# Kernel tuning notes

Measured on AMD Instinct MI355X. Metric: run time of the kernel, lower is better.

The kernel has to match this reference:

```python
import jax, jax.numpy as jnp
import numpy as np

LEAKY_SLOPE = 0.2  # PyG GATConv default negative_slope
EPS = 1e-16


def _gat_layer(h_in, src, dst, W, a_src, a_dst, b, concat):
    # h_in: [N, Fin]; src/dst: [Etot] (self-loops included); W: [Fin, H*C]
    N = h_in.shape[0]
    H, C = a_src.shape
    h = (h_in @ W).reshape(N, H, C)                       # [N,H,C]
    al_s = jnp.sum(h * a_src, axis=-1)                    # [N,H]
    al_d = jnp.sum(h * a_dst, axis=-1)                    # [N,H]
    e = jax.nn.leaky_relu(al_s[src] + al_d[dst], LEAKY_SLOPE)  # [E,H]
    emax = jax.ops.segment_max(e, dst, num_segments=N)    # segment softmax over dst
    p = jnp.exp(e - emax[dst])
    denom = jax.ops.segment_sum(p, dst, num_segments=N)
    alpha = p / (denom[dst] + EPS)                        # [E,H]
    out = jax.ops.segment_sum(h[src] * alpha[:, :, None], dst, num_segments=N)  # [N,H,C]
    out = out.reshape(N, H * C) if concat else out.mean(axis=1)
    return out + b


def setup_inputs() -> dict:
    key = jax.random.key(0)
    ks = jax.random.split(key, 16)
    N, E, Fin, Hd, Hh = 10000, 320000, 256, 128, 4

    def glorot(k, shape, fan_in):
        return jax.random.normal(k, shape, dtype=jnp.float32) * (1.0 / np.sqrt(fan_in))

    inp = {
        "x": jax.random.normal(ks[0], (N, Fin), dtype=jnp.float32),
        "edge_index": jax.random.randint(ks[1], (2, E), 0, N, dtype=jnp.int32),
        # conv1: Fin -> Hd x Hh heads, concat
        "W1": glorot(ks[2], (Fin, Hh * Hd), Fin),
        "a1_src": glorot(ks[3], (Hh, Hd), Hd),
        "a1_dst": glorot(ks[4], (Hh, Hd), Hd),
        "b1": jnp.zeros((Hh * Hd,), jnp.float32),
        # conv2: Hh*Hd -> Hd x Hh heads, concat
        "W2": glorot(ks[5], (Hh * Hd, Hh * Hd), Hh * Hd),
        "a2_src": glorot(ks[6], (Hh, Hd), Hd),
        "a2_dst": glorot(ks[7], (Hh, Hd), Hd),
        "b2": jnp.zeros((Hh * Hd,), jnp.float32),
        # conv3: Hh*Hd -> Hd, 1 head, concat=False (mean)
        "W3": glorot(ks[8], (Hh * Hd, Hd), Hh * Hd),
        "a3_src": glorot(ks[9], (1, Hd), Hd),
        "a3_dst": glorot(ks[10], (1, Hd), Hd),
        "b3": jnp.zeros((Hd,), jnp.float32),
        # classifier: Hd -> Hd//2 -> 2
        "Wc1": glorot(ks[11], (Hd, Hd // 2), Hd),
        "bc1": jnp.zeros((Hd // 2,), jnp.float32),
        "Wc2": glorot(ks[12], (Hd // 2, 2), Hd // 2),
        "bc2": jnp.zeros((2,), jnp.float32),
    }
    return inp


def reference(x, edge_index, W1, a1_src, a1_dst, b1, W2, a2_src, a2_dst, b2,
              W3, a3_src, a3_dst, b3, Wc1, bc1, Wc2, bc2):
    N = x.shape[0]
    loops = jnp.arange(N, dtype=edge_index.dtype)
    src = jnp.concatenate([edge_index[0], loops])  # PyG adds self-loops
    dst = jnp.concatenate([edge_index[1], loops])

    h = jax.nn.elu(_gat_layer(x, src, dst, W1, a1_src, a1_dst, b1, concat=True))
    h = jax.nn.elu(_gat_layer(h, src, dst, W2, a2_src, a2_dst, b2, concat=True))
    embeddings = _gat_layer(h, src, dst, W3, a3_src, a3_dst, b3, concat=False)  # [N, 128]
    out = jax.nn.relu(embeddings @ Wc1 + bc1) @ Wc2 + bc2  # [N, 2]
    return out, embeddings
```

## Files before the change

### kernel.cpp

```cpp
#include <hip/hip_runtime.h>
#include <cstddef>

#define LEAKY 0.2f
#define EPS_DEN 1e-16f

typedef short bf8_t __attribute__((ext_vector_type(8)));
typedef float f4_t __attribute__((ext_vector_type(4)));
typedef unsigned short us2_t __attribute__((ext_vector_type(2)));

__device__ __forceinline__ unsigned short f2bf(float f) {
    unsigned u = __float_as_uint(f);
    unsigned r = (u + 0x7fffu + ((u >> 16) & 1u)) >> 16;
    return (unsigned short)r;
}
__device__ __forceinline__ float bf2f(unsigned short h) {
    return __uint_as_float(((unsigned)h) << 16);
}

__global__ void hist_kernel(const int* __restrict__ dst, int* __restrict__ counts, int E) {
    int i = blockIdx.x * blockDim.x + threadIdx.x;
    if (i < E) atomicAdd(&counts[dst[i]], 1);
}

__global__ void scan1_kernel(int* __restrict__ cnt, int* __restrict__ bsum, int N) {
    __shared__ int s[256];
    int t = threadIdx.x;
    int i = blockIdx.x * 256 + t;
    int v = (i < N) ? cnt[i] : 0;
    s[t] = v;
    __syncthreads();
#pragma unroll
    for (int st = 1; st < 256; st <<= 1) {
        int add = (t >= st) ? s[t - st] : 0;
        __syncthreads();
        s[t] += add;
        __syncthreads();
    }
    if (i < N) cnt[i] = s[t] - v;
    if (t == 255) bsum[blockIdx.x] = s[255];
}

__global__ void scan2_kernel(int* __restrict__ bsum, int* __restrict__ offs, int NB, int N) {
    int t = threadIdx.x;
    int v = (t < NB) ? bsum[t] : 0;
    int inc = v;
#pragma unroll
    for (int off = 1; off < 64; off <<= 1) {
        int u = __shfl_up(inc, off);
        if (t >= off) inc += u;
    }
    if (t < NB) bsum[t] = inc - v;
    if (t == 63) offs[N] = inc;
}

__global__ void scan3_kernel(int* __restrict__ cnt, const int* __restrict__ bsum,
                             int* __restrict__ offs, int N) {
    int i = blockIdx.x * 256 + threadIdx.x;
    if (i < N) {
        int o = cnt[i] + bsum[blockIdx.x];
        offs[i] = o;
        cnt[i] = o;
    }
}

__global__ void scatter_kernel(const int* __restrict__ src, const int* __restrict__ dst,
                               int* __restrict__ cursor, int* __restrict__ csrc, int E) {
    int i = blockIdx.x * blockDim.x + threadIdx.x;
    if (i < E) {
        int d = dst[i];
        int pos = atomicAdd(&cursor[d], 1);
        csrc[pos] = src[i];
    }
}

__global__ void split_kernel(const float* __restrict__ in, unsigned short* __restrict__ hi,
                             unsigned short* __restrict__ lo, int len) {
    int i = blockIdx.x * blockDim.x + threadIdx.x;
    if (i >= len) return;
    float v = in[i];
    unsigned short h = f2bf(v);
    hi[i] = h;
    lo[i] = f2bf(v - bf2f(h));
}

__global__ void wsplit_kernel(const float* __restrict__ W, unsigned short* __restrict__ hi,
                              unsigned short* __restrict__ lo, int K, int N) {
    int idx = blockIdx.x * blockDim.x + threadIdx.x;
    if (idx >= K * N) return;
    int n = idx / K, k = idx % K;
    float v = W[(size_t)k * N + n];
    unsigned short h = f2bf(v);
    hi[idx] = h;
    lo[idx] = f2bf(v - bf2f(h));
}

__global__ __launch_bounds__(256) void mfma_gemm_kernel(
    const unsigned short* __restrict__ Ahi, const unsigned short* __restrict__ Alo,
    const unsigned short* __restrict__ BThi, const unsigned short* __restrict__ BTlo,
    float* __restrict__ C, int M, int N, int K) {
    constexpr int BK = 32;
    __shared__ __align__(16) unsigned short sA[128 * BK];
    __shared__ __align__(16) unsigned short sB[128 * BK];
    int t = threadIdx.x;
    int w = t >> 6, lane = t & 63;
    int quad = lane >> 4, low = lane & 15;
    int m0 = blockIdx.y * 128, n0 = blockIdx.x * 128;
    int wm = (w & 1) * 64, wn = (w >> 1) * 64;

    f4_t acc[4][4];
#pragma unroll
    for (int i = 0; i < 4; i++)
#pragma unroll
        for (int j = 0; j < 4; j++) acc[i][j] = (f4_t){0.f, 0.f, 0.f, 0.f};

    int srow = lane >> 2;
    int schunk = lane & 3;

    const unsigned short* Ap[3] = {Ahi, Ahi, Alo};
    const unsigned short* Bp[3] = {BThi, BTlo, BThi};

    for (int pass = 0; pass < 3; pass++) {
        const unsigned short* A = Ap[pass];
        const unsigned short* B = Bp[pass];
        for (int k0 = 0; k0 < K; k0 += BK) {
            __syncthreads();
#pragma unroll
            for (int inst = 0; inst < 2; inst++) {
                int r = w * 32 + inst * 16 + srow;
                int gm = m0 + r;
                if (gm >= M) gm = M - 1;
                const void* g = (const void*)(A + (size_t)gm * K + k0 + schunk * 8);
                void* l = (void*)((char*)sA + (size_t)(w * 2048 + inst * 1024));
                __builtin_amdgcn_global_load_lds((const __attribute__((address_space(1))) void*)g,
                                                 (__attribute__((address_space(3))) void*)l, 16, 0, 0);
            }
#pragma unroll
            for (int inst = 0; inst < 2; inst++) {
                int r = w * 32 + inst * 16 + srow;
                int gn = n0 + r;
                const void* g = (const void*)(B + (size_t)gn * K + k0 + schunk * 8);
                void* l = (void*)((char*)sB + (size_t)(w * 2048 + inst * 1024));
                __builtin_amdgcn_global_load_lds((const __attribute__((address_space(1))) void*)g,
                                                 (__attribute__((address_space(3))) void*)l, 16, 0, 0);
            }
            __syncthreads();

            bf8_t af[4], bf[4];
#pragma unroll
            for (int i = 0; i < 4; i++) {
                int row = wm + i * 16 + low;
                af[i] = *(const bf8_t*)&sA[row * BK + quad * 8];
            }
#pragma unroll
            for (int j = 0; j < 4; j++) {
                int row = wn + j * 16 + low;
                bf[j] = *(const bf8_t*)&sB[row * BK + quad * 8];
            }
#pragma unroll
            for (int i = 0; i < 4; i++)
#pragma unroll
                for (int j = 0; j < 4; j++)
                    acc[i][j] = __builtin_amdgcn_mfma_f32_16x16x32_bf16(af[i], bf[j], acc[i][j], 0, 0, 0);
        }
    }

#pragma unroll
    for (int i = 0; i < 4; i++) {
#pragma unroll
        for (int r = 0; r < 4; r++) {
            int gm = m0 + wm + i * 16 + quad * 4 + r;
            if (gm >= M) continue;
#pragma unroll
            for (int j = 0; j < 4; j++) {
                int gn = n0 + wn + j * 16 + low;
                C[(size_t)gm * N + gn] = acc[i][j][r];
            }
        }
    }
}

__global__ void al_h4_kernel(const float* __restrict__ h, const float* __restrict__ a_src,
                             const float* __restrict__ a_dst, float* __restrict__ als,
                             float* __restrict__ ald, int N) {
    int wave = threadIdx.x >> 6, lane = threadIdx.x & 63;
    int n = blockIdx.x * 4 + wave;
    if (n >= N) return;
    const float* row = h + (size_t)n * 512;
    float ps[4] = {0, 0, 0, 0}, pd[4] = {0, 0, 0, 0};
#pragma unroll
    for (int k = 0; k < 8; k++) {
        int f = k * 64 + lane;
        float v = row[f];
        ps[k >> 1] += v * a_src[f];
        pd[k >> 1] += v * a_dst[f];
    }
#pragma unroll
    for (int off = 32; off; off >>= 1) {
#pragma unroll
        for (int hd = 0; hd < 4; hd++) {
            ps[hd] += __shfl_down(ps[hd], off);
            pd[hd] += __shfl_down(pd[hd], off);
        }
    }
    if (lane == 0) {
#pragma unroll
        for (int hd = 0; hd < 4; hd++) {
            als[n * 4 + hd] = ps[hd];
            ald[n * 4 + hd] = pd[hd];
        }
    }
}

__global__ void al_h1_kernel(const float* __restrict__ h, const float* __restrict__ a_src,
                             const float* __restrict__ a_dst, float* __restrict__ als,
                             float* __restrict__ ald, int N) {
    int wave = threadIdx.x >> 6, lane = threadIdx.x & 63;
    int n = blockIdx.x * 4 + wave;
    if (n >= N) return;
    const float* row = h + (size_t)n * 128;
    float v0 = row[lane], v1 = row[lane + 64];
    float ps = v0 * a_src[lane] + v1 * a_src[lane + 64];
    float pd = v0 * a_dst[lane] + v1 * a_dst[lane + 64];
#pragma unroll
    for (int off = 32; off; off >>= 1) {
        ps += __shfl_down(ps, off);
        pd += __shfl_down(pd, off);
    }
    if (lane == 0) { als[n] = ps; ald[n] = pd; }
}

__global__ void stats_h4_kernel(const int* __restrict__ csrc, const int* __restrict__ offs,
                                const float* __restrict__ als, const float* __restrict__ ald,
                                float* __restrict__ pbuf, float* __restrict__ psf, int N, int E) {
    int wave = threadIdx.x >> 6, lane = threadIdx.x & 63;
    int n = blockIdx.x * 4 + wave;
    if (n >= N) return;
    int hd = lane & 3, es = lane >> 2;
    float aldn = ald[n * 4 + hd];
    float selfe = als[n * 4 + hd] + aldn;
    selfe = selfe > 0.f ? selfe : LEAKY * selfe;
    int beg = offs[n], end = offs[n + 1];
    float* pb = pbuf + (size_t)hd * E;
    float m = selfe;
    for (int base = beg; base + es < end; base += 16) {
        int idx = base + es;
        int s = csrc[idx];
        float e = als[s * 4 + hd] + aldn;
        e = e > 0.f ? e : LEAKY * e;
        pb[idx] = e;
        m = fmaxf(m, e);
    }
#pragma unroll
    for (int off = 4; off < 64; off <<= 1) m = fmaxf(m, __shfl_xor(m, off));
    float d = 0.f;
    for (int base = beg; base + es < end; base += 16) {
        int idx = base + es;
        float p = __expf(pb[idx] - m);
        pb[idx] = p;
        d += p;
    }
#pragma unroll
    for (int off = 4; off < 64; off <<= 1) d += __shfl_xor(d, off);
    float pself = __expf(selfe - m);
    float r = 1.0f / (d + pself + EPS_DEN);
    if (es == 0) psf[n * 4 + hd] = pself * r;
    for (int base = beg; base + es < end; base += 16) {
        int idx = base + es;
        pb[idx] *= r;
    }
}

__global__ void stats_h1_kernel(const int* __restrict__ csrc, const int* __restrict__ offs,
                                const float* __restrict__ als, const float* __restrict__ ald,
                                float* __restrict__ pbuf, float* __restrict__ psf, int N) {
    int wave = threadIdx.x >> 6, lane = threadIdx.x & 63;
    int n = blockIdx.x * 4 + wave;
    if (n >= N) return;
    float aldn = ald[n];
    float selfe = als[n] + aldn;
    selfe = selfe > 0.f ? selfe : LEAKY * selfe;
    int beg = offs[n], end = offs[n + 1];
    float m = selfe;
    for (int base = beg; base + lane < end; base += 64) {
        int idx = base + lane;
        int s = csrc[idx];
        float e = als[s] + aldn;
        e = e > 0.f ? e : LEAKY * e;
        pbuf[idx] = e;
        m = fmaxf(m, e);
    }
#pragma unroll
    for (int off = 1; off < 64; off <<= 1) m = fmaxf(m, __shfl_xor(m, off));
    float d = 0.f;
    for (int base = beg; base + lane < end; base += 64) {
        int idx = base + lane;
        float p = __expf(pbuf[idx] - m);
        pbuf[idx] = p;
        d += p;
    }
#pragma unroll
    for (int off = 1; off < 64; off <<= 1) d += __shfl_xor(d, off);
    float pself = __expf(selfe - m);
    float r = 1.0f / (d + pself + EPS_DEN);
    if (lane == 0) psf[n] = pself * r;
    for (int base = beg; base + lane < end; base += 64) {
        int idx = base + lane;
        pbuf[idx] *= r;
    }
}

template <bool DO_ELU>
__global__ __launch_bounds__(64) void gat_aggregate_h4_kernel(
    const float* __restrict__ h, const float* __restrict__ pbuf,
    const float* __restrict__ psf, const int* __restrict__ csrc,
    const int* __restrict__ offs, const float* __restrict__ bias,
    unsigned short* __restrict__ ohi, unsigned short* __restrict__ olo, int N, int E) {
    int gid = blockIdx.x;
    int head = gid & 3;
    int n = gid >> 2;
    int lane = threadIdx.x;
    int f0 = head * 128 + lane * 2;
    const float* selfrow = h + (size_t)n * 512;
    const float* pb = pbuf + (size_t)head * E;
    float a0, a1;
    {
        float pself = psf[n * 4 + head];
        a0 = pself * selfrow[f0];
        a1 = pself * selfrow[f0 + 1];
    }
    __shared__ int sSrc[64];
    __shared__ float sP[64];
    int beg = offs[n], end = offs[n + 1];
    for (int base = beg; base < end; base += 64) {
        int len = min(64, end - base);
        __syncthreads();
        if (lane < len) {
            sSrc[lane] = csrc[base + lane];
            sP[lane] = pb[base + lane];
        }
        __syncthreads();
#pragma unroll 4
        for (int c = 0; c < len; c++) {
            const float* srow = h + (size_t)sSrc[c] * 512;
            float p = sP[c];
            float2 x = *(const float2*)(srow + f0);
            a0 += p * x.x;
            a1 += p * x.y;
        }
    }
    a0 += bias[f0];
    a1 += bias[f0 + 1];
    if (DO_ELU) {
        a0 = a0 > 0.f ? a0 : (__expf(a0) - 1.0f);
        a1 = a1 > 0.f ? a1 : (__expf(a1) - 1.0f);
    }
    size_t idx = (size_t)n * 512 + f0;
    us2_t hs, ls;
    unsigned short h0 = f2bf(a0), h1 = f2bf(a1);
    hs[0] = h0; hs[1] = h1;
    ls[0] = f2bf(a0 - bf2f(h0)); ls[1] = f2bf(a1 - bf2f(h1));
    *(us2_t*)&ohi[idx] = hs;
    *(us2_t*)&olo[idx] = ls;
}

template <int NT, int VEC>
__global__ void gat_aggregate_h1_kernel(const float* __restrict__ h, const float* __restrict__ pbuf,
                                        const float* __restrict__ psf, const int* __restrict__ csrc,
                                        const int* __restrict__ offs, const float* __restrict__ bias,
                                        float* __restrict__ outp, int N) {
    constexpr int F = 128;
    constexpr int CH = 64;
    __shared__ int sSrc[CH];
    __shared__ float sP[CH];
    int n = blockIdx.x;
    int t = threadIdx.x;
    int f0 = t * VEC;
    const float* selfrow = h + (size_t)n * F;
    float acc[VEC];
    {
        float pself = psf[n];
#pragma unroll
        for (int j = 0; j < VEC; j++) acc[j] = pself * selfrow[f0 + j];
    }
    int beg = offs[n], end = offs[n + 1];
    for (int base = beg; base < end; base += CH) {
        int len = min(CH, end - base);
        __syncthreads();
        for (int c = t; c < len; c += NT) {
            sSrc[c] = csrc[base + c];
            sP[c] = pbuf[base + c];
        }
        __syncthreads();
#pragma unroll 4
        for (int c = 0; c < len; c++) {
            const float* srow = h + (size_t)sSrc[c] * F;
            float p = sP[c];
            using vec_t = float __attribute__((ext_vector_type(VEC)));
            vec_t x = *(const vec_t*)(srow + f0);
#pragma unroll
            for (int j = 0; j < VEC; j++) acc[j] += p * x[j];
        }
    }
#pragma unroll
    for (int j = 0; j < VEC; j++) outp[(size_t)n * F + f0 + j] = acc[j] + bias[f0 + j];
}

__global__ void classifier_kernel(const float* __restrict__ emb, const float* __restrict__ Wc1,
                                  const float* __restrict__ bc1, const float* __restrict__ Wc2,
                                  const float* __restrict__ bc2, float* __restrict__ out, int N) {
    int wave = threadIdx.x >> 6, lane = threadIdx.x & 63;
    int n = blockIdx.x * 4 + wave;
    if (n >= N) return;
    const float* row = emb + (size_t)n * 128;
    float acc = bc1[lane];
#pragma unroll 4
    for (int k = 0; k < 128; k++) acc += row[k] * Wc1[k * 64 + lane];
    acc = fmaxf(acc, 0.f);
    float o0 = acc * Wc2[lane * 2 + 0];
    float o1 = acc * Wc2[lane * 2 + 1];
#pragma unroll
    for (int off = 32; off; off >>= 1) {
        o0 += __shfl_down(o0, off);
        o1 += __shfl_down(o1, off);
    }
    if (lane == 0) {
        out[n * 2 + 0] = o0 + bc2[0];
        out[n * 2 + 1] = o1 + bc2[1];
    }
}

extern "C" void kernel_launch(void* const* d_in, const int* in_sizes, int n_in,
                              void* d_out, int out_size, void* d_ws, size_t ws_size,
                              hipStream_t stream) {
    const float* x      = (const float*)d_in[0];
    const int*   ei     = (const int*)d_in[1];
    const float* W1     = (const float*)d_in[2];
    const float* a1s    = (const float*)d_in[3];
    const float* a1d    = (const float*)d_in[4];
    const float* b1     = (const float*)d_in[5];
    const float* W2     = (const float*)d_in[6];
    const float* a2s    = (const float*)d_in[7];
    const float* a2d    = (const float*)d_in[8];
    const float* b2     = (const float*)d_in[9];
    const float* W3     = (const float*)d_in[10];
    const float* a3s    = (const float*)d_in[11];
    const float* a3d    = (const float*)d_in[12];
    const float* b3     = (const float*)d_in[13];
    const float* Wc1    = (const float*)d_in[14];
    const float* bc1    = (const float*)d_in[15];
    const float* Wc2    = (const float*)d_in[16];
    const float* bc2    = (const float*)d_in[17];

    const int N = in_sizes[0] / 256;
    const int E = in_sizes[1] / 2;
    const int F = 512;

    const int* src = ei;
    const int* dst = ei + E;

    auto align = [](size_t o) { return (o + 255) & ~(size_t)255; };
    size_t o = 0;
    size_t o_G     = o; o = align(o + (size_t)N * F * 4);
    size_t o_ahi   = o; o = align(o + (size_t)N * F * 2);
    size_t o_alo   = o; o = align(o + (size_t)N * F * 2);
    size_t o_xhi   = o; o = align(o + (size_t)N * 256 * 2);
    size_t o_xlo   = o; o = align(o + (size_t)N * 256 * 2);
    size_t o_w1h   = o; o = align(o + (size_t)512 * 256 * 2);
    size_t o_w1l   = o; o = align(o + (size_t)512 * 256 * 2);
    size_t o_w2h   = o; o = align(o + (size_t)512 * 512 * 2);
    size_t o_w2l   = o; o = align(o + (size_t)512 * 512 * 2);
    size_t o_w3h   = o; o = align(o + (size_t)128 * 512 * 2);
    size_t o_w3l   = o; o = align(o + (size_t)128 * 512 * 2);
    size_t o_als   = o; o = align(o + (size_t)N * 4 * 4);
    size_t o_ald   = o; o = align(o + (size_t)N * 4 * 4);
    size_t o_psf   = o; o = align(o + (size_t)N * 4 * 4);
    size_t o_cnt   = o; o = align(o + (size_t)N * 4);
    size_t o_off   = o; o = align(o + (size_t)(N + 1) * 4);
    size_t o_bsum  = o; o = align(o + (size_t)64 * 4);
    size_t o_csrc  = o; o = align(o + (size_t)E * 4);
    size_t o_ebuf  = o; o = align(o + (size_t)E * 4 * 4);
    (void)ws_size;

    char* ws = (char*)d_ws;
    float* bufG  = (float*)(ws + o_G);
    unsigned short* act_hi = (unsigned short*)(ws + o_ahi);
    unsigned short* act_lo = (unsigned short*)(ws + o_alo);
    unsigned short* x_hi   = (unsigned short*)(ws + o_xhi);
    unsigned short* x_lo   = (unsigned short*)(ws + o_xlo);
    unsigned short* w1h = (unsigned short*)(ws + o_w1h);
    unsigned short* w1l = (unsigned short*)(ws + o_w1l);
    unsigned short* w2h = (unsigned short*)(ws + o_w2h);
    unsigned short* w2l = (unsigned short*)(ws + o_w2l);
    unsigned short* w3h = (unsigned short*)(ws + o_w3h);
    unsigned short* w3l = (unsigned short*)(ws + o_w3l);
    float* als  = (float*)(ws + o_als);
    float* ald  = (float*)(ws + o_ald);
    float* psf  = (float*)(ws + o_psf);
    int*   cnt  = (int*)(ws + o_cnt);
    int*   offs = (int*)(ws + o_off);
    int*   bsum = (int*)(ws + o_bsum);
    int*   csrc = (int*)(ws + o_csrc);
    float* ebuf = (float*)(ws + o_ebuf);

    float* outp = (float*)d_out;
    float* emb  = (float*)d_out + (size_t)N * 2;

    hipMemsetAsync(cnt, 0, (size_t)N * 4, stream);
    int eb = (E + 255) / 256;
    int nbs = (N + 255) / 256;
    hipLaunchKernelGGL(hist_kernel, dim3(eb), dim3(256), 0, stream, dst, cnt, E);
    hipLaunchKernelGGL(scan1_kernel, dim3(nbs), dim3(256), 0, stream, cnt, bsum, N);
    hipLaunchKernelGGL(scan2_kernel, dim3(1), dim3(64), 0, stream, bsum, offs, nbs, N);
    hipLaunchKernelGGL(scan3_kernel, dim3(nbs), dim3(256), 0, stream, cnt, bsum, offs, N);
    hipLaunchKernelGGL(scatter_kernel, dim3(eb), dim3(256), 0, stream, src, dst, cnt, csrc, E);

    hipLaunchKernelGGL(split_kernel, dim3((N * 256 + 255) / 256), dim3(256), 0, stream,
                       x, x_hi, x_lo, N * 256);
    hipLaunchKernelGGL(wsplit_kernel, dim3((256 * 512 + 255) / 256), dim3(256), 0, stream,
                       W1, w1h, w1l, 256, 512);
    hipLaunchKernelGGL(wsplit_kernel, dim3((512 * 512 + 255) / 256), dim3(256), 0, stream,
                       W2, w2h, w2l, 512, 512);
    hipLaunchKernelGGL(wsplit_kernel, dim3((512 * 128 + 255) / 256), dim3(256), 0, stream,
                       W3, w3h, w3l, 512, 128);

    int nb4 = (N + 3) / 4;
    int gy  = (N + 127) / 128;

    hipLaunchKernelGGL(mfma_gemm_kernel, dim3(512 / 128, gy), dim3(256), 0, stream,
                       x_hi, x_lo, w1h, w1l, bufG, N, 512, 256);
    hipLaunchKernelGGL(al_h4_kernel, dim3(nb4), dim3(256), 0, stream, bufG, a1s, a1d, als, ald, N);
    hipLaunchKernelGGL(stats_h4_kernel, dim3(nb4), dim3(256), 0, stream,
                       csrc, offs, als, ald, ebuf, psf, N, E);
    hipLaunchKernelGGL((gat_aggregate_h4_kernel<true>), dim3(N * 4), dim3(64), 0, stream,
                       bufG, ebuf, psf, csrc, offs, b1, act_hi, act_lo, N, E);

    hipLaunchKernelGGL(mfma_gemm_kernel, dim3(512 / 128, gy), dim3(256), 0, stream,
                       act_hi, act_lo, w2h, w2l, bufG, N, 512, 512);
    hipLaunchKernelGGL(al_h4_kernel, dim3(nb4), dim3(256), 0, stream, bufG, a2s, a2d, als, ald, N);
    hipLaunchKernelGGL(stats_h4_kernel, dim3(nb4), dim3(256), 0, stream,
                       csrc, offs, als, ald, ebuf, psf, N, E);
    hipLaunchKernelGGL((gat_aggregate_h4_kernel<true>), dim3(N * 4), dim3(64), 0, stream,
                       bufG, ebuf, psf, csrc, offs, b2, act_hi, act_lo, N, E);

    hipLaunchKernelGGL(mfma_gemm_kernel, dim3(128 / 128, gy), dim3(256), 0, stream,
                       act_hi, act_lo, w3h, w3l, bufG, N, 128, 512);
    hipLaunchKernelGGL(al_h1_kernel, dim3(nb4), dim3(256), 0, stream, bufG, a3s, a3d, als, ald, N);
    hipLaunchKernelGGL(stats_h1_kernel, dim3(nb4), dim3(256), 0, stream,
                       csrc, offs, als, ald, ebuf, psf, N);
    hipLaunchKernelGGL((gat_aggregate_h1_kernel<64, 2>), dim3(N), dim3(64), 0, stream,
                       bufG, ebuf, psf, csrc, offs, b3, emb, N);

    hipLaunchKernelGGL(classifier_kernel, dim3(nb4), dim3(256), 0, stream,
                       emb, Wc1, bc1, Wc2, bc2, outp, N);
}
```

Measured before the change: 421.3 us.

## Shrink GEMM M-tile, defer softmax normalization, vectorize aggregation with half-wave split

Three separate changes. The GEMM tile shrinks from 128x128 to 64x128, doubling the number of blocks so a 10000-row problem fills more compute units, at the cost of less reuse per block. The stats kernels no longer make a third pass over the edges to normalize probabilities; they store the self-loop weight and the reciprocal denominator, and the aggregation kernels apply that scale once at the end. The aggregation kernels now use 4-wide vector loads and split alternate edges between the two halves of the wave, combining the partial sums with a cross-lane shuffle. This exposes more memory parallelism per node, at the cost of one extra reduction step.

New measurement: 397.4 us. 5.7% less time.

```diff
diff --git a/kernel.cpp b/kernel.cpp
--- a/kernel.cpp
+++ b/kernel.cpp
@@ -6,7 +6,7 @@
 
 typedef short bf8_t __attribute__((ext_vector_type(8)));
 typedef float f4_t __attribute__((ext_vector_type(4)));
-typedef unsigned short us2_t __attribute__((ext_vector_type(2)));
+typedef unsigned short us4_t __attribute__((ext_vector_type(4)));
 
 __device__ __forceinline__ unsigned short f2bf(float f) {
     unsigned u = __float_as_uint(f);
@@ -99,17 +99,17 @@
     const unsigned short* __restrict__ BThi, const unsigned short* __restrict__ BTlo,
     float* __restrict__ C, int M, int N, int K) {
     constexpr int BK = 32;
-    __shared__ __align__(16) unsigned short sA[128 * BK];
+    __shared__ __align__(16) unsigned short sA[64 * BK];
     __shared__ __align__(16) unsigned short sB[128 * BK];
     int t = threadIdx.x;
     int w = t >> 6, lane = t & 63;
     int quad = lane >> 4, low = lane & 15;
-    int m0 = blockIdx.y * 128, n0 = blockIdx.x * 128;
-    int wm = (w & 1) * 64, wn = (w >> 1) * 64;
-
-    f4_t acc[4][4];
-#pragma unroll
-    for (int i = 0; i < 4; i++)
+    int m0 = blockIdx.y * 64, n0 = blockIdx.x * 128;
+    int wm = (w & 1) * 32, wn = (w >> 1) * 64;
+
+    f4_t acc[2][4];
+#pragma unroll
+    for (int i = 0; i < 2; i++)
 #pragma unroll
         for (int j = 0; j < 4; j++) acc[i][j] = (f4_t){0.f, 0.f, 0.f, 0.f};
 
@@ -124,20 +124,17 @@
         const unsigned short* B = Bp[pass];
         for (int k0 = 0; k0 < K; k0 += BK) {
             __syncthreads();
-#pragma unroll
-            for (int inst = 0; inst < 2; inst++) {
-                int r = w * 32 + inst * 16 + srow;
-                int gm = m0 + r;
+            {
+                int gm = m0 + w * 16 + srow;
                 if (gm >= M) gm = M - 1;
                 const void* g = (const void*)(A + (size_t)gm * K + k0 + schunk * 8);
-                void* l = (void*)((char*)sA + (size_t)(w * 2048 + inst * 1024));
+                void* l = (void*)((char*)sA + (size_t)(w * 1024));
                 __builtin_amdgcn_global_load_lds((const __attribute__((address_space(1))) void*)g,
                                                  (__attribute__((address_space(3))) void*)l, 16, 0, 0);
             }
 #pragma unroll
             for (int inst = 0; inst < 2; inst++) {
-                int r = w * 32 + inst * 16 + srow;
-                int gn = n0 + r;
+                int gn = n0 + w * 32 + inst * 16 + srow;
                 const void* g = (const void*)(B + (size_t)gn * K + k0 + schunk * 8);
                 void* l = (void*)((char*)sB + (size_t)(w * 2048 + inst * 1024));
                 __builtin_amdgcn_global_load_lds((const __attribute__((address_space(1))) void*)g,
@@ -145,9 +142,9 @@
             }
             __syncthreads();
 
-            bf8_t af[4], bf[4];
-#pragma unroll
-            for (int i = 0; i < 4; i++) {
+            bf8_t af[2], bf[4];
+#pragma unroll
+            for (int i = 0; i < 2; i++) {
                 int row = wm + i * 16 + low;
                 af[i] = *(const bf8_t*)&sA[row * BK + quad * 8];
             }
@@ -157,7 +154,7 @@
                 bf[j] = *(const bf8_t*)&sB[row * BK + quad * 8];
             }
 #pragma unroll
-            for (int i = 0; i < 4; i++)
+            for (int i = 0; i < 2; i++)
 #pragma unroll
                 for (int j = 0; j < 4; j++)
                     acc[i][j] = __builtin_amdgcn_mfma_f32_16x16x32_bf16(af[i], bf[j], acc[i][j], 0, 0, 0);
@@ -165,7 +162,7 @@
     }
 
 #pragma unroll
-    for (int i = 0; i < 4; i++) {
+    for (int i = 0; i < 2; i++) {
 #pragma unroll
         for (int r = 0; r < 4; r++) {
             int gm = m0 + wm + i * 16 + quad * 4 + r;
@@ -231,7 +228,8 @@
 
 __global__ void stats_h4_kernel(const int* __restrict__ csrc, const int* __restrict__ offs,
                                 const float* __restrict__ als, const float* __restrict__ ald,
-                                float* __restrict__ pbuf, float* __restrict__ psf, int N, int E) {
+                                float* __restrict__ pbuf, float* __restrict__ psf,
+                                float* __restrict__ rden, int N, int E) {
     int wave = threadIdx.x >> 6, lane = threadIdx.x & 63;
     int n = blockIdx.x * 4 + wave;
     if (n >= N) return;
@@ -263,16 +261,16 @@
     for (int off = 4; off < 64; off <<= 1) d += __shfl_xor(d, off);
     float pself = __expf(selfe - m);
     float r = 1.0f / (d + pself + EPS_DEN);
-    if (es == 0) psf[n * 4 + hd] = pself * r;
-    for (int base = beg; base + es < end; base += 16) {
-        int idx = base + es;
-        pb[idx] *= r;
+    if (es == 0) {
+        psf[n * 4 + hd] = pself;
+        rden[n * 4 + hd] = r;
     }
 }
 
 __global__ void stats_h1_kernel(const int* __restrict__ csrc, const int* __restrict__ offs,
                                 const float* __restrict__ als, const float* __restrict__ ald,
-                                float* __restrict__ pbuf, float* __restrict__ psf, int N) {
+                                float* __restrict__ pbuf, float* __restrict__ psf,
+                                float* __restrict__ rden, int N) {
     int wave = threadIdx.x >> 6, lane = threadIdx.x & 63;
     int n = blockIdx.x * 4 + wave;
     if (n >= N) return;
@@ -302,31 +300,29 @@
     for (int off = 1; off < 64; off <<= 1) d += __shfl_xor(d, off);
     float pself = __expf(selfe - m);
     float r = 1.0f / (d + pself + EPS_DEN);
-    if (lane == 0) psf[n] = pself * r;
-    for (int base = beg; base + lane < end; base += 64) {
-        int idx = base + lane;
-        pbuf[idx] *= r;
-    }
+    if (lane == 0) { psf[n] = pself; rden[n] = r; }
 }
 
 template <bool DO_ELU>
 __global__ __launch_bounds__(64) void gat_aggregate_h4_kernel(
     const float* __restrict__ h, const float* __restrict__ pbuf,
-    const float* __restrict__ psf, const int* __restrict__ csrc,
-    const int* __restrict__ offs, const float* __restrict__ bias,
-    unsigned short* __restrict__ ohi, unsigned short* __restrict__ olo, int N, int E) {
+    const float* __restrict__ psf, const float* __restrict__ rden,
+    const int* __restrict__ csrc, const int* __restrict__ offs,
+    const float* __restrict__ bias, unsigned short* __restrict__ ohi,
+    unsigned short* __restrict__ olo, int N, int E) {
     int gid = blockIdx.x;
     int head = gid & 3;
     int n = gid >> 2;
     int lane = threadIdx.x;
-    int f0 = head * 128 + lane * 2;
-    const float* selfrow = h + (size_t)n * 512;
+    int half = lane >> 5;
+    int fl = (lane & 31) * 4;
+    int f0 = head * 128 + fl;
     const float* pb = pbuf + (size_t)head * E;
-    float a0, a1;
+    f4_t acc;
     {
-        float pself = psf[n * 4 + head];
-        a0 = pself * selfrow[f0];
-        a1 = pself * selfrow[f0 + 1];
+        float pself = (half == 0) ? psf[n * 4 + head] : 0.f;
+        f4_t x = *(const f4_t*)(h + (size_t)n * 512 + f0);
+        acc = pself * x;
     }
     __shared__ int sSrc[64];
     __shared__ float sP[64];
@@ -339,70 +335,78 @@
             sP[lane] = pb[base + lane];
         }
         __syncthreads();
-#pragma unroll 4
-        for (int c = 0; c < len; c++) {
+#pragma unroll 8
+        for (int c = half; c < len; c += 2) {
             const float* srow = h + (size_t)sSrc[c] * 512;
             float p = sP[c];
-            float2 x = *(const float2*)(srow + f0);
-            a0 += p * x.x;
-            a1 += p * x.y;
-        }
-    }
-    a0 += bias[f0];
-    a1 += bias[f0 + 1];
-    if (DO_ELU) {
-        a0 = a0 > 0.f ? a0 : (__expf(a0) - 1.0f);
-        a1 = a1 > 0.f ? a1 : (__expf(a1) - 1.0f);
-    }
-    size_t idx = (size_t)n * 512 + f0;
-    us2_t hs, ls;
-    unsigned short h0 = f2bf(a0), h1 = f2bf(a1);
-    hs[0] = h0; hs[1] = h1;
-    ls[0] = f2bf(a0 - bf2f(h0)); ls[1] = f2bf(a1 - bf2f(h1));
-    *(us2_t*)&ohi[idx] = hs;
-    *(us2_t*)&olo[idx] = ls;
-}
-
-template <int NT, int VEC>
-__global__ void gat_aggregate_h1_kernel(const float* __restrict__ h, const float* __restrict__ pbuf,
-                                        const float* __restrict__ psf, const int* __restrict__ csrc,
-                                        const int* __restrict__ offs, const float* __restrict__ bias,
-                                        float* __restrict__ outp, int N) {
-    constexpr int F = 128;
-    constexpr int CH = 64;
-    __shared__ int sSrc[CH];
-    __shared__ float sP[CH];
+            f4_t x = *(const f4_t*)(srow + f0);
+            acc += p * x;
+        }
+    }
+#pragma unroll
+    for (int j = 0; j < 4; j++) acc[j] += __shfl_xor(acc[j], 32);
+    float r = rden[n * 4 + head];
+    f4_t b = *(const f4_t*)(bias + f0);
+    us4_t hs, ls;
+#pragma unroll
+    for (int j = 0; j < 4; j++) {
+        float o = acc[j] * r + b[j];
+        if (DO_ELU) o = o > 0.f ? o : (__expf(o) - 1.0f);
+        unsigned short hh = f2bf(o);
+        hs[j] = hh;
+        ls[j] = f2bf(o - bf2f(hh));
+    }
+    if (half == 0) {
+        size_t idx = (size_t)n * 512 + f0;
+        *(us4_t*)&ohi[idx] = hs;
+        *(us4_t*)&olo[idx] = ls;
+    }
+}
+
+__global__ __launch_bounds__(64) void gat_aggregate_h1_kernel(
+    const float* __restrict__ h, const float* __restrict__ pbuf,
+    const float* __restrict__ psf, const float* __restrict__ rden,
+    const int* __restrict__ csrc, const int* __restrict__ offs,
+    const float* __restrict__ bias, float* __restrict__ outp, int N) {
     int n = blockIdx.x;
-    int t = threadIdx.x;
-    int f0 = t * VEC;
-    const float* selfrow = h + (size_t)n * F;
-    float acc[VEC];
+    int lane = threadIdx.x;
+    int half = lane >> 5;
+    int f0 = (lane & 31) * 4;
+    f4_t acc;
     {
-        float pself = psf[n];
-#pragma unroll
-        for (int j = 0; j < VEC; j++) acc[j] = pself * selfrow[f0 + j];
-    }
+        float pself = (half == 0) ? psf[n] : 0.f;
+        f4_t x = *(const f4_t*)(h + (size_t)n * 128 + f0);
+        acc = pself * x;
+    }
+    __shared__ int sSrc[64];
+    __shared__ float sP[64];
     int beg = offs[n], end = offs[n + 1];
-    for (int base = beg; base < end; base += CH) {
-        int len = min(CH, end - base);
+    for (int base = beg; base < end; base += 64) {
+        int len = min(64, end - base);
         __syncthreads();
-        for (int c = t; c < len; c += NT) {
-            sSrc[c] = csrc[base + c];
-            sP[c] = pbuf[base + c];
+        if (lane < len) {
+            sSrc[lane] = csrc[base + lane];
+            sP[lane] = pbuf[base + lane];
         }
         __syncthreads();
-#pragma unroll 4
-        for (int c = 0; c < len; c++) {
-            const float* srow = h + (size_t)sSrc[c] * F;
+#pragma unroll 8
+        for (int c = half; c < len; c += 2) {
+            const float* srow = h + (size_t)sSrc[c] * 128;
             float p = sP[c];
-            using vec_t = float __attribute__((ext_vector_type(VEC)));
-            vec_t x = *(const vec_t*)(srow + f0);
-#pragma unroll
-            for (int j = 0; j < VEC; j++) acc[j] += p * x[j];
-        }
-    }
-#pragma unroll
-    for (int j = 0; j < VEC; j++) outp[(size_t)n * F + f0 + j] = acc[j] + bias[f0 + j];
+            f4_t x = *(const f4_t*)(srow + f0);
+            acc += p * x;
+        }
+    }
+#pragma unroll
+    for (int j = 0; j < 4; j++) acc[j] += __shfl_xor(acc[j], 32);
+    if (half == 0) {
+        float r = rden[n];
+        f4_t b = *(const f4_t*)(bias + f0);
+        f4_t o;
+#pragma unroll
+        for (int j = 0; j < 4; j++) o[j] = acc[j] * r + b[j];
+        *(f4_t*)&outp[(size_t)n * 128 + f0] = o;
+    }
 }
 
 __global__ void classifier_kernel(const float* __restrict__ emb, const float* __restrict__ Wc1,
@@ -474,6 +478,7 @@
     size_t o_als   = o; o = align(o + (size_t)N * 4 * 4);
     size_t o_ald   = o; o = align(o + (size_t)N * 4 * 4);
     size_t o_psf   = o; o = align(o + (size_t)N * 4 * 4);
+    size_t o_rden  = o; o = align(o + (size_t)N * 4 * 4);
     size_t o_cnt   = o; o = align(o + (size_t)N * 4);
     size_t o_off   = o; o = align(o + (size_t)(N + 1) * 4);
     size_t o_bsum  = o; o = align(o + (size_t)64 * 4);
@@ -496,6 +501,7 @@
     float* als  = (float*)(ws + o_als);
     float* ald  = (float*)(ws + o_ald);
     float* psf  = (float*)(ws + o_psf);
+    float* rden = (float*)(ws + o_rden);
     int*   cnt  = (int*)(ws + o_cnt);
     int*   offs = (int*)(ws + o_off);
     int*   bsum = (int*)(ws + o_bsum);
@@ -524,31 +530,31 @@
                        W3, w3h, w3l, 512, 128);
 
     int nb4 = (N + 3) / 4;
-    int gy  = (N + 127) / 128;
+    int gy  = (N + 63) / 64;
 
     hipLaunchKernelGGL(mfma_gemm_kernel, dim3(512 / 128, gy), dim3(256), 0, stream,
                        x_hi, x_lo, w1h, w1l, bufG, N, 512, 256);
     hipLaunchKernelGGL(al_h4_kernel, dim3(nb4), dim3(256), 0, stream, bufG, a1s, a1d, als, ald, N);
     hipLaunchKernelGGL(stats_h4_kernel, dim3(nb4), dim3(256), 0, stream,
-                       csrc, offs, als, ald, ebuf, psf, N, E);
+                       csrc, offs, als, ald, ebuf, psf, rden, N, E);
     hipLaunchKernelGGL((gat_aggregate_h4_kernel<true>), dim3(N * 4), dim3(64), 0, stream,
-                       bufG, ebuf, psf, csrc, offs, b1, act_hi, act_lo, N, E);
+                       bufG, ebuf, psf, rden, csrc, offs, b1, act_hi, act_lo, N, E);
 
     hipLaunchKernelGGL(mfma_gemm_kernel, dim3(512 / 128, gy), dim3(256), 0, stream,
                        act_hi, act_lo, w2h, w2l, bufG, N, 512, 512);
     hipLaunchKernelGGL(al_h4_kernel, dim3(nb4), dim3(256), 0, stream, bufG, a2s, a2d, als, ald, N);
     hipLaunchKernelGGL(stats_h4_kernel, dim3(nb4), dim3(256), 0, stream,
-                       csrc, offs, als, ald, ebuf, psf, N, E);
+                       csrc, offs, als, ald, ebuf, psf, rden, N, E);
     hipLaunchKernelGGL((gat_aggregate_h4_kernel<true>), dim3(N * 4), dim3(64), 0, stream,
-                       bufG, ebuf, psf, csrc, offs, b2, act_hi, act_lo, N, E);
+                       bufG, ebuf, psf, rden, csrc, offs, b2, act_hi, act_lo, N, E);
 
     hipLaunchKernelGGL(mfma_gemm_kernel, dim3(128 / 128, gy), dim3(256), 0, stream,
                        act_hi, act_lo, w3h, w3l, bufG, N, 128, 512);
     hipLaunchKernelGGL(al_h1_kernel, dim3(nb4), dim3(256), 0, stream, bufG, a3s, a3d, als, ald, N);
     hipLaunchKernelGGL(stats_h1_kernel, dim3(nb4), dim3(256), 0, stream,
-                       csrc, offs, als, ald, ebuf, psf, N);
-    hipLaunchKernelGGL((gat_aggregate_h1_kernel<64, 2>), dim3(N), dim3(64), 0, stream,
-                       bufG, ebuf, psf, csrc, offs, b3, emb, N);
+                       csrc, offs, als, ald, ebuf, psf, rden, N);
+    hipLaunchKernelGGL(gat_aggregate_h1_kernel, dim3(N), dim3(64), 0, stream,
+                       bufG, ebuf, psf, rden, csrc, offs, b3, emb, N);
 
     hipLaunchKernelGGL(classifier_kernel, dim3(nb4), dim3(256), 0, stream,
                        emb, Wc1, bc1, Wc2, bc2, outp, N);
```
